# Optimization experiments

Measured on AMD Instinct MI355X. Metric: run time of the kernel, lower is better.

## Reference

```python
import jax, jax.numpy as jnp
import numpy as np
from jax import lax

DN = ('NCHW', 'OIHW', 'NCHW')


def setup_inputs() -> dict:
    key = jax.random.key(0)
    k1, k2 = jax.random.split(key)
    x = jax.random.uniform(k1, (32, 3, 128, 128), dtype=jnp.float32)
    # kaiming-uniform-like filters; the module zeroes the first filter after init
    fan_in = 1 * 7 * 7
    bound = np.sqrt(6.0 / ((1 + 5.0) * fan_in))  # kaiming_uniform with a=sqrt(5)
    weight = jax.random.uniform(k2, (512, 1, 7, 7), minval=-bound, maxval=bound,
                                dtype=jnp.float32)
    weight = weight.at[0].set(0.0)
    std = jnp.asarray(2.0, dtype=jnp.float32)
    return {"x": x, "weight": weight, "std": std}


def _rbf_dist_conv(gray, weight, std, stride=1):
    # ||window - filter||^2 = ||window||^2 + ||filter||^2 - 2 * window . filter
    strides = (stride, stride)
    xw = lax.conv_general_dilated(gray, weight, strides, 'VALID',
                                  dimension_numbers=DN)       # [B,O,OH,OW]
    ones_k = jnp.ones((1, 1) + weight.shape[2:], gray.dtype)
    x2 = lax.conv_general_dilated(gray * gray, ones_k, strides, 'VALID',
                                  dimension_numbers=DN)       # [B,1,OH,OW]
    w2 = jnp.sum(weight * weight, axis=(1, 2, 3))[None, :, None, None]
    sq = jnp.maximum(x2 + w2 - 2.0 * xw, 0.0)
    dist = jnp.sqrt(sq)                                        # torch.cdist
    # gauss RBF: exp(-d^2 / (2*std^2))
    return jnp.exp(-(dist * dist) / (2.0 * std * std))


def reference(x, weight, std):
    # forward converts 3-channel input to grayscale (ITU-R 601 weights, as torchvision)
    gray = (0.2989 * x[:, 0] + 0.587 * x[:, 1] + 0.114 * x[:, 2])[:, None]  # [B,1,H,W]
    return _rbf_dist_conv(gray, weight, std, stride=1)
```

## Files before the change

kernel.cpp:

```cpp
#include <hip/hip_runtime.h>

typedef _Float16 half_t;
typedef __attribute__((ext_vector_type(4))) _Float16 half4;
typedef __attribute__((ext_vector_type(8))) _Float16 half8;
typedef __attribute__((ext_vector_type(2))) float f32x2;
typedef __attribute__((ext_vector_type(4))) float f32x4;

#define NB 32
#define NH 128
#define NW 128
#define NOH 122
#define NOW 122
#define NOC 512
#define KPAD 64


__global__ __launch_bounds__(256) void k_gray(const float* __restrict__ x,
                                              half_t* __restrict__ gh) {
    int t = blockIdx.x * 256 + threadIdx.x;
    if (t >= NB * NH * NW / 4) return;
    int b = t >> 12;
    int pix4 = t & 4095;
    const float* xb = x + (size_t)b * 3 * 16384 + pix4 * 4;
    f32x4 r = *(const f32x4*)xb;
    f32x4 g = *(const f32x4*)(xb + 16384);
    f32x4 bl = *(const f32x4*)(xb + 32768);
    half4 o;
#pragma unroll
    for (int i = 0; i < 4; ++i)
        o[i] = (half_t)(0.2989f * r[i] + 0.587f * g[i] + 0.114f * bl[i]);
    *(half4*)(gh + (size_t)t * 4) = o;
}

__global__ __launch_bounds__(64) void k_w(const float* __restrict__ w,
                                          half_t* __restrict__ Wh,
                                          float* __restrict__ w2) {
    int o = blockIdx.x * 64 + threadIdx.x;
    if (o >= NOC) return;
    float s = 0.f;
    for (int t = 0; t < KPAD; ++t) {
        int kh = t >> 3, kw = t & 7;
        float v = (kh < 7 && kw < 7) ? w[o * 49 + kh * 7 + kw] : 0.f;
        half_t h = (half_t)v;
        Wh[o * KPAD + t] = h;
        float f = (float)h;
        s += f * f;
    }
    w2[o] = s;
}

__global__ __launch_bounds__(256) void k_rs(const half_t* __restrict__ gh,
                                            float* __restrict__ Sg) {
    int t = blockIdx.x * 256 + threadIdx.x;
    if (t >= NB * NH * NOW) return;
    int b = t / (NH * NOW);
    int rem = t - b * (NH * NOW);
    int h = rem / NOW;
    int p = rem - h * NOW;
    const half_t* g = gh + ((size_t)b * NH + h) * NW + p;
    float s = 0.f;
#pragma unroll
    for (int kw = 0; kw < 7; ++kw) {
        float v = (float)g[kw];
        s += v * v;
    }
    Sg[t] = s;
}

__global__ __launch_bounds__(256) void k_x2(const float* __restrict__ Sg,
                                            float* __restrict__ x2) {
    int t = blockIdx.x * 256 + threadIdx.x;
    if (t >= NB * NOH * NOW) return;
    int b = t / (NOH * NOW);
    int rem = t - b * (NOH * NOW);
    int oh = rem / NOW;
    int p = rem - oh * NOW;
    const float* s0 = Sg + ((size_t)b * NH + oh) * NOW + p;
    float s = 0.f;
#pragma unroll
    for (int kh = 0; kh < 7; ++kh) s += s0[kh * NOW];
    x2[t] = s;
}

__global__ __launch_bounds__(256, 2) void k_main(const half_t* __restrict__ gh,
                                                 const half_t* __restrict__ Wh,
                                                 const float* __restrict__ w2,
                                                 const float* __restrict__ x2,
                                                 const float* __restrict__ stdp,
                                                 float* __restrict__ out) {
    const int fg  = blockIdx.x;
    const int ohp = blockIdx.y;
    const int b   = blockIdx.z;
    const int oh0 = ohp * 2;

    __shared__ half_t gS[9][136];
    __shared__ float  outT[64 * 244];

    const int tid  = threadIdx.x;
    const int wave = tid >> 6;
    const int lane = tid & 63;
    const int col  = lane & 15;
    const int kq   = lane >> 4;
    const int n0   = wave * 32;

    for (int idx = tid; idx < 9 * 136; idx += 256) {
        int r = idx / 136;
        int c = idx - r * 136;
        int row = oh0 + r;
        if (row > NH - 1) row = NH - 1;
        gS[r][c] = (c < 128) ? gh[((size_t)b * NH + row) * NW + c] : (half_t)0.f;
    }

    half8 wfrag[4][2];
#pragma unroll
    for (int ni = 0; ni < 4; ++ni)
#pragma unroll
        for (int ks = 0; ks < 2; ++ks)
            wfrag[ni][ks] = *(const half8*)(Wh + ((size_t)(fg * 64 + ni * 16 + col) * KPAD
                                                  + (ks * 4 + kq) * 8));
    float w2c[4];
#pragma unroll
    for (int ni = 0; ni < 4; ++ni) w2c[ni] = w2[fg * 64 + ni * 16 + col];

    const float sv = stdp[0];
    const float inv2s2 = 0.5f / (sv * sv);

    __syncthreads();

#pragma unroll
    for (int lo = 0; lo < 2; ++lo) {
        const int oh = oh0 + lo;

        half8 afrag[2][2];
#pragma unroll
        for (int mi = 0; mi < 2; ++mi) {
            const int p = n0 + mi * 16 + col;
#pragma unroll
            for (int ks = 0; ks < 2; ++ks) {
                const half_t* src = &gS[lo + ks * 4 + kq][p];
                half8 v;
#pragma unroll
                for (int i = 0; i < 8; ++i) v[i] = src[i];
                afrag[mi][ks] = v;
            }
        }

        f32x4 acc[2][4];
#pragma unroll
        for (int mi = 0; mi < 2; ++mi)
#pragma unroll
            for (int ni = 0; ni < 4; ++ni) {
                f32x4 z = {0.f, 0.f, 0.f, 0.f};
                acc[mi][ni] = z;
            }

#pragma unroll
        for (int ks = 0; ks < 2; ++ks)
#pragma unroll
            for (int mi = 0; mi < 2; ++mi)
#pragma unroll
                for (int ni = 0; ni < 4; ++ni)
                    acc[mi][ni] = __builtin_amdgcn_mfma_f32_16x16x32_f16(
                        afrag[mi][ks], wfrag[ni][ks], acc[mi][ni], 0, 0, 0);

        const size_t rowBase = ((size_t)b * NOH + oh) * NOW;

#pragma unroll
        for (int mi = 0; mi < 2; ++mi) {
            const int p0 = n0 + mi * 16 + kq * 4;
            if (p0 >= NOW) continue;
            const f32x4 x2v = *(const f32x4*)(x2 + rowBase + p0);
            const bool full = (p0 + 3 < NOW);
#pragma unroll
            for (int ni = 0; ni < 4; ++ni) {
                f32x4 res;
#pragma unroll
                for (int r = 0; r < 4; ++r) {
                    float sq = fmaxf(fmaf(-2.f, acc[mi][ni][r], x2v[r] + w2c[ni]), 0.f);
                    res[r] = __expf(-sq * inv2s2);
                }
                float* dst = &outT[(ni * 16 + col) * 244 + lo * 122 + p0];
                f32x2 lo2 = {res[0], res[1]};
                *(f32x2*)dst = lo2;
                if (full) {
                    f32x2 hi2 = {res[2], res[3]};
                    *(f32x2*)(dst + 2) = hi2;
                }
            }
        }
    }

    __syncthreads();

    if (lane < 61) {
        const size_t base = (((size_t)b * NOC + fg * 64) * NOH + oh0) * NOW;
#pragma unroll 4
        for (int c = 0; c < 16; ++c) {
            const int o = wave * 16 + c;
            f32x4 v = *(const f32x4*)&outT[o * 244 + lane * 4];
            *(f32x4*)(out + base + (size_t)o * NOH * NOW + lane * 4) = v;
        }
    }
}

extern "C" void kernel_launch(void* const* d_in, const int* in_sizes, int n_in,
                              void* d_out, int out_size, void* d_ws, size_t ws_size,
                              hipStream_t stream) {
    const float* x    = (const float*)d_in[0];
    const float* w    = (const float*)d_in[1];
    const float* stdp = (const float*)d_in[2];
    float* out = (float*)d_out;

    char* ws = (char*)d_ws;
    half_t* gh = (half_t*)ws;
    half_t* Wh = (half_t*)(ws + 1048576);
    float*  w2 = (float*)(ws + 1114112);
    float*  x2 = (float*)(ws + 1116160);
    float*  Sg = (float*)(ws + 3021440);

    k_gray<<<(NB * NH * NW / 4 + 255) / 256, 256, 0, stream>>>(x, gh);
    k_w<<<(NOC + 63) / 64, 64, 0, stream>>>(w, Wh, w2);
    k_rs<<<(NB * NH * NOW + 255) / 256, 256, 0, stream>>>(gh, Sg);
    k_x2<<<(NB * NOH * NOW + 255) / 256, 256, 0, stream>>>(Sg, x2);

    dim3 grid(8, 61, NB);
    k_main<<<grid, 256, 0, stream>>>(gh, Wh, w2, x2, stdp, out);
}
```

Baseline: 314.5 us.

## Fuse window-energy computation into main kernel and halve filter tile per block

Removes the two separate kernels that built the per-window squared-sum (x2) through a global intermediate. Each main block now computes row sums and 7-row column sums from its shared-memory gray tile. Filters per block drop from 64 to 32, which halves the output staging buffer, and the grid doubles along the filter axis with a higher occupancy hint. The cost is x2 being recomputed redundantly by the 16 filter-group blocks that share each row pair, plus two extra barriers per block.

```diff
diff --git a/kernel.cpp b/kernel.cpp
--- a/kernel.cpp
+++ b/kernel.cpp
@@ -32,10 +32,10 @@
     *(half4*)(gh + (size_t)t * 4) = o;
 }
 
-__global__ __launch_bounds__(64) void k_w(const float* __restrict__ w,
-                                          half_t* __restrict__ Wh,
-                                          float* __restrict__ w2) {
-    int o = blockIdx.x * 64 + threadIdx.x;
+__global__ __launch_bounds__(256) void k_w(const float* __restrict__ w,
+                                           half_t* __restrict__ Wh,
+                                           float* __restrict__ w2) {
+    int o = blockIdx.x * 256 + threadIdx.x;
     if (o >= NOC) return;
     float s = 0.f;
     for (int t = 0; t < KPAD; ++t) {
@@ -49,52 +49,20 @@
     w2[o] = s;
 }
 
-__global__ __launch_bounds__(256) void k_rs(const half_t* __restrict__ gh,
-                                            float* __restrict__ Sg) {
-    int t = blockIdx.x * 256 + threadIdx.x;
-    if (t >= NB * NH * NOW) return;
-    int b = t / (NH * NOW);
-    int rem = t - b * (NH * NOW);
-    int h = rem / NOW;
-    int p = rem - h * NOW;
-    const half_t* g = gh + ((size_t)b * NH + h) * NW + p;
-    float s = 0.f;
-#pragma unroll
-    for (int kw = 0; kw < 7; ++kw) {
-        float v = (float)g[kw];
-        s += v * v;
-    }
-    Sg[t] = s;
-}
-
-__global__ __launch_bounds__(256) void k_x2(const float* __restrict__ Sg,
-                                            float* __restrict__ x2) {
-    int t = blockIdx.x * 256 + threadIdx.x;
-    if (t >= NB * NOH * NOW) return;
-    int b = t / (NOH * NOW);
-    int rem = t - b * (NOH * NOW);
-    int oh = rem / NOW;
-    int p = rem - oh * NOW;
-    const float* s0 = Sg + ((size_t)b * NH + oh) * NOW + p;
-    float s = 0.f;
-#pragma unroll
-    for (int kh = 0; kh < 7; ++kh) s += s0[kh * NOW];
-    x2[t] = s;
-}
-
-__global__ __launch_bounds__(256, 2) void k_main(const half_t* __restrict__ gh,
+__global__ __launch_bounds__(256, 4) void k_main(const half_t* __restrict__ gh,
                                                  const half_t* __restrict__ Wh,
                                                  const float* __restrict__ w2,
-                                                 const float* __restrict__ x2,
                                                  const float* __restrict__ stdp,
                                                  float* __restrict__ out) {
-    const int fg  = blockIdx.x;
+    const int fgg = blockIdx.x;
     const int ohp = blockIdx.y;
     const int b   = blockIdx.z;
     const int oh0 = ohp * 2;
 
     __shared__ half_t gS[9][136];
-    __shared__ float  outT[64 * 244];
+    __shared__ float  rs2[8][124];
+    __shared__ float  x2L[2][124];
+    __shared__ float  outT[32 * 244];
 
     const int tid  = threadIdx.x;
     const int wave = tid >> 6;
@@ -111,26 +79,53 @@
         gS[r][c] = (c < 128) ? gh[((size_t)b * NH + row) * NW + c] : (half_t)0.f;
     }
 
-    half8 wfrag[4][2];
-#pragma unroll
-    for (int ni = 0; ni < 4; ++ni)
+    half8 wfrag[2][2];
+#pragma unroll
+    for (int ni = 0; ni < 2; ++ni)
 #pragma unroll
         for (int ks = 0; ks < 2; ++ks)
-            wfrag[ni][ks] = *(const half8*)(Wh + ((size_t)(fg * 64 + ni * 16 + col) * KPAD
+            wfrag[ni][ks] = *(const half8*)(Wh + ((size_t)(fgg * 32 + ni * 16 + col) * KPAD
                                                   + (ks * 4 + kq) * 8));
-    float w2c[4];
-#pragma unroll
-    for (int ni = 0; ni < 4; ++ni) w2c[ni] = w2[fg * 64 + ni * 16 + col];
+    float w2c[2];
+#pragma unroll
+    for (int ni = 0; ni < 2; ++ni) w2c[ni] = w2[fgg * 32 + ni * 16 + col];
 
     const float sv = stdp[0];
     const float inv2s2 = 0.5f / (sv * sv);
 
     __syncthreads();
 
+    for (int idx = tid; idx < 8 * 128; idx += 256) {
+        int r = idx >> 7;
+        int p = idx & 127;
+        if (p < NOW) {
+            float s = 0.f;
+#pragma unroll
+            for (int kw = 0; kw < 7; ++kw) {
+                float v = (float)gS[r][p + kw];
+                s += v * v;
+            }
+            rs2[r][p] = s;
+        }
+    }
+    __syncthreads();
+
+    if (tid < 256) {
+        int lo = tid >> 7;
+        int p = tid & 127;
+        if (p < 124) {
+            float s = 0.f;
+            if (p < NOW) {
+#pragma unroll
+                for (int kh = 0; kh < 7; ++kh) s += rs2[lo + kh][p];
+            }
+            x2L[lo][p] = s;
+        }
+    }
+    __syncthreads();
+
 #pragma unroll
     for (int lo = 0; lo < 2; ++lo) {
-        const int oh = oh0 + lo;
-
         half8 afrag[2][2];
 #pragma unroll
         for (int mi = 0; mi < 2; ++mi) {
@@ -145,11 +140,11 @@
             }
         }
 
-        f32x4 acc[2][4];
+        f32x4 acc[2][2];
 #pragma unroll
         for (int mi = 0; mi < 2; ++mi)
 #pragma unroll
-            for (int ni = 0; ni < 4; ++ni) {
+            for (int ni = 0; ni < 2; ++ni) {
                 f32x4 z = {0.f, 0.f, 0.f, 0.f};
                 acc[mi][ni] = z;
             }
@@ -159,20 +154,18 @@
 #pragma unroll
             for (int mi = 0; mi < 2; ++mi)
 #pragma unroll
-                for (int ni = 0; ni < 4; ++ni)
+                for (int ni = 0; ni < 2; ++ni)
                     acc[mi][ni] = __builtin_amdgcn_mfma_f32_16x16x32_f16(
                         afrag[mi][ks], wfrag[ni][ks], acc[mi][ni], 0, 0, 0);
-
-        const size_t rowBase = ((size_t)b * NOH + oh) * NOW;
 
 #pragma unroll
         for (int mi = 0; mi < 2; ++mi) {
             const int p0 = n0 + mi * 16 + kq * 4;
             if (p0 >= NOW) continue;
-            const f32x4 x2v = *(const f32x4*)(x2 + rowBase + p0);
+            const f32x4 x2v = *(const f32x4*)(&x2L[lo][p0]);
             const bool full = (p0 + 3 < NOW);
 #pragma unroll
-            for (int ni = 0; ni < 4; ++ni) {
+            for (int ni = 0; ni < 2; ++ni) {
                 f32x4 res;
 #pragma unroll
                 for (int r = 0; r < 4; ++r) {
@@ -193,10 +186,10 @@
     __syncthreads();
 
     if (lane < 61) {
-        const size_t base = (((size_t)b * NOC + fg * 64) * NOH + oh0) * NOW;
+        const size_t base = (((size_t)b * NOC + fgg * 32) * NOH + oh0) * NOW;
 #pragma unroll 4
-        for (int c = 0; c < 16; ++c) {
-            const int o = wave * 16 + c;
+        for (int c = 0; c < 8; ++c) {
+            const int o = wave * 8 + c;
             f32x4 v = *(const f32x4*)&outT[o * 244 + lane * 4];
             *(f32x4*)(out + base + (size_t)o * NOH * NOW + lane * 4) = v;
         }
@@ -215,14 +208,10 @@
     half_t* gh = (half_t*)ws;
     half_t* Wh = (half_t*)(ws + 1048576);
     float*  w2 = (float*)(ws + 1114112);
-    float*  x2 = (float*)(ws + 1116160);
-    float*  Sg = (float*)(ws + 3021440);
 
     k_gray<<<(NB * NH * NW / 4 + 255) / 256, 256, 0, stream>>>(x, gh);
-    k_w<<<(NOC + 63) / 64, 64, 0, stream>>>(w, Wh, w2);
-    k_rs<<<(NB * NH * NOW + 255) / 256, 256, 0, stream>>>(gh, Sg);
-    k_x2<<<(NB * NOH * NOW + 255) / 256, 256, 0, stream>>>(Sg, x2);
-
-    dim3 grid(8, 61, NB);
-    k_main<<<grid, 256, 0, stream>>>(gh, Wh, w2, x2, stdp, out);
-}
+    k_w<<<(NOC + 255) / 256, 256, 0, stream>>>(w, Wh, w2);
+
+    dim3 grid(16, 61, NB);
+    k_main<<<grid, 256, 0, stream>>>(gh, Wh, w2, stdp, out);
+}
```

Measured after the change: 356.5 us. 13.4% more time.
